# Performance work log

Hardware: AMD Instinct MI355X
Metric: run time of the kernel (lower is better)

Reference implementation:

```python
import jax, jax.numpy as jnp
import numpy as np

NUM_HEADS = 8
HEAD_SIZE = 64  # hidden_dim // num_heads = 512 // 8
SCALE = 1.0 / np.sqrt(HEAD_SIZE).astype(np.float32)
CAUSAL = True


def setup_inputs() -> dict:
    key = jax.random.key(0)
    k1, k2, k3 = jax.random.split(key, 3)
    b, s, d = 4, 2048, 512
    x = jax.random.normal(k1, (b, s, d), dtype=jnp.float32)
    w_qkv = jax.random.normal(k2, (d, 3 * d), dtype=jnp.float32) * 0.02
    b_qkv = jnp.zeros((3 * d,), dtype=jnp.float32)
    w_out = jax.random.normal(k3, (d, d), dtype=jnp.float32) * 0.02
    b_out = jnp.zeros((d,), dtype=jnp.float32)
    return {"x": x, "w_qkv": w_qkv, "b_qkv": b_qkv, "w_out": w_out, "b_out": b_out}


def reference(x, w_qkv, b_qkv, w_out, b_out):
    b, s, d = x.shape
    h, hd = NUM_HEADS, HEAD_SIZE
    qkv = x @ w_qkv + b_qkv                      # (b, s, 3d)
    q, k, v = jnp.split(qkv, 3, axis=-1)
    # (b, s, d) -> (b, h, s, hd)
    q = q.reshape(b, s, h, hd).transpose(0, 2, 1, 3)
    k = k.reshape(b, s, h, hd).transpose(0, 2, 1, 3)
    v = v.reshape(b, s, h, hd).transpose(0, 2, 1, 3)
    scores = jnp.einsum('bhqd,bhkd->bhqk', q, k) * SCALE  # (b, h, s, s)
    if CAUSAL:
        causal_mask = jnp.triu(jnp.ones((s, s), dtype=bool), k=1)
        scores = jnp.where(causal_mask, -jnp.inf, scores)
    attn = jax.nn.softmax(scores, axis=-1)
    out = jnp.einsum('bhqk,bhkd->bhqd', attn, v)          # (b, h, s, hd)
    out = out.transpose(0, 2, 1, 3).reshape(b, s, d)
    return out @ w_out + b_out
```

## Files before the change

kernel.cpp:

```cpp
#include <hip/hip_runtime.h>
#include <hip/hip_bf16.h>

#define BATCH 4
#define SEQ   2048
#define DM    512
#define NH    8
#define HD    64
#define PART  (BATCH*NH*SEQ*HD)
#define QSCALE 0.18033688f

typedef unsigned short u16;
typedef unsigned int   u32;
typedef __bf16 bf16x8 __attribute__((ext_vector_type(8)));
typedef float  f32x4  __attribute__((ext_vector_type(4)));

__device__ __forceinline__ u16 f2bf(float f) {
    union { float f; u32 u; } v; v.f = f;
    u32 r = v.u + 0x7fffu + ((v.u >> 16) & 1u);
    return (u16)(r >> 16);
}

__device__ __forceinline__ void glds16(const u16* g, u16* lds) {
    __builtin_amdgcn_global_load_lds(
        (const __attribute__((address_space(1))) void*)g,
        (__attribute__((address_space(3))) void*)lds, 16, 0, 0);
}

__global__ __launch_bounds__(256) void prep_k(
    const float* __restrict__ x, u16* __restrict__ xb,
    const float* __restrict__ w_qkv, u16* __restrict__ t_qkv,
    const float* __restrict__ w_out, u16* __restrict__ t_out)
{
    __shared__ u16 Ts[64][72];
    const int z = blockIdx.z, bx = blockIdx.x, t = threadIdx.x;

    if (z == 0) {
        const int n8 = PART / 8;
        for (int i = bx * 256 + t; i < n8; i += 512 * 256) {
            float4 a = *(const float4*)(x + (size_t)i * 8);
            float4 b = *(const float4*)(x + (size_t)i * 8 + 4);
            union { uint4 v; u16 s[8]; } o;
            o.s[0] = f2bf(a.x); o.s[1] = f2bf(a.y);
            o.s[2] = f2bf(a.z); o.s[3] = f2bf(a.w);
            o.s[4] = f2bf(b.x); o.s[5] = f2bf(b.y);
            o.s[6] = f2bf(b.z); o.s[7] = f2bf(b.w);
            *(uint4*)(xb + (size_t)i * 8) = o.v;
        }
        return;
    }
    const int N = (z == 1) ? 3 * DM : DM;
    const int ntiles = N / 64;
    if (bx >= ntiles * 8) return;
    const float* W = (z == 1) ? w_qkv : w_out;
    u16* Wt = (z == 1) ? t_qkv : t_out;
    const int n0 = (bx % ntiles) * 64, k0 = (bx / ntiles) * 64;

    #pragma unroll
    for (int l = 0; l < 4; ++l) {
        int idx = l * 1024 + t * 4;
        int r = idx >> 6, c = idx & 63;
        float4 v = *(const float4*)(W + (size_t)(k0 + r) * N + n0 + c);
        Ts[c + 0][r] = f2bf(v.x);
        Ts[c + 1][r] = f2bf(v.y);
        Ts[c + 2][r] = f2bf(v.z);
        Ts[c + 3][r] = f2bf(v.w);
    }
    __syncthreads();
    #pragma unroll
    for (int l = 0; l < 2; ++l) {
        int idx = l * 256 + t;
        int row = idx >> 3, ch = idx & 7;
        *(uint4*)(Wt + (size_t)(n0 + row) * DM + k0 + ch * 8) =
            *(const uint4*)(&Ts[row][ch * 8]);
    }
}

template<int MODE>
__global__ __launch_bounds__(256) void gemm_k(
    const u16* __restrict__ A, const u16* __restrict__ Bt,
    const float* __restrict__ bias, void* __restrict__ outv,
    int M, int N, int K)
{
    constexpr int BM = (MODE == 1) ? 64 : 128;
    constexpr int NI = (MODE == 1) ? 2 : 4;

    __shared__ __align__(16) u16 As[2][BM * 32];
    __shared__ __align__(16) u16 Bs[2][128 * 32];
    __shared__ __align__(16) u16 epi[128 * 72];

    const int tid  = threadIdx.x;
    const int bm0  = blockIdx.x * BM;
    const int bn0  = blockIdx.y * 128;
    const int wave = tid >> 6, lane = tid & 63;
    const int l16  = lane & 15, quad = lane >> 4;
    const int wr   = (MODE == 1) ? 0 : (wave & 1) * 64;
    const int wc   = (MODE == 1) ? wave * 32 : (wave >> 1) * 64;

    const int srow = (lane >> 2);
    const int scol = (lane & 3) * 8;
    const int arow = (MODE == 1) ? (wave * 16) : (wave * 32);
    const u16* Ag = A + (size_t)(bm0 + arow + srow) * K + scol;
    const u16* Bg = Bt + (size_t)(bn0 + wave * 32 + srow) * K + scol;
    const int wofsA = arow * 32;
    const int wofsB = (wave * 32) * 32;

    f32x4 acc[4][NI];
    #pragma unroll
    for (int i = 0; i < 4; ++i)
        #pragma unroll
        for (int j = 0; j < NI; ++j)
            acc[i][j] = (f32x4){0.f, 0.f, 0.f, 0.f};

    glds16(Ag, &As[0][wofsA]);
    if (MODE == 0) glds16(Ag + (size_t)16 * K, &As[0][wofsA + 16 * 32]);
    glds16(Bg,                  &Bs[0][wofsB]);
    glds16(Bg + (size_t)16 * K, &Bs[0][wofsB + 16 * 32]);
    __syncthreads();

    const int NIT = K >> 5;
    for (int it = 0; it < NIT; ++it) {
        const int cur = it & 1;
        if (it + 1 < NIT) {
            const int nx = cur ^ 1;
            const int k0 = (it + 1) << 5;
            glds16(Ag + k0, &As[nx][wofsA]);
            if (MODE == 0) glds16(Ag + k0 + (size_t)16 * K, &As[nx][wofsA + 16 * 32]);
            glds16(Bg + k0,                  &Bs[nx][wofsB]);
            glds16(Bg + k0 + (size_t)16 * K, &Bs[nx][wofsB + 16 * 32]);
        }

        bf16x8 af[4], bfr[NI];
        #pragma unroll
        for (int mi = 0; mi < 4; ++mi)
            af[mi] = *(const bf16x8*)(&As[cur][(wr + mi * 16 + l16) * 32 + quad * 8]);
        #pragma unroll
        for (int ni = 0; ni < NI; ++ni)
            bfr[ni] = *(const bf16x8*)(&Bs[cur][(wc + ni * 16 + l16) * 32 + quad * 8]);
        #pragma unroll
        for (int mi = 0; mi < 4; ++mi)
            #pragma unroll
            for (int ni = 0; ni < NI; ++ni)
                acc[mi][ni] = __builtin_amdgcn_mfma_f32_16x16x32_bf16(
                    af[mi], bfr[ni], acc[mi][ni], 0, 0, 0);
        __syncthreads();
    }

    if (MODE == 1) {
        #pragma unroll
        for (int mi = 0; mi < 4; ++mi)
            #pragma unroll
            for (int ni = 0; ni < NI; ++ni) {
                int col = bn0 + wc + ni * 16 + l16;
                float bv = bias[col];
                int row0 = bm0 + wr + mi * 16 + quad * 4;
                #pragma unroll
                for (int reg = 0; reg < 4; ++reg)
                    ((float*)outv)[(size_t)(row0 + reg) * N + col] =
                        acc[mi][ni][reg] + bv;
            }
    } else {
        u16* ws = (u16*)outv;
        const int part = bn0 >> 9;
        const int h0   = (bn0 & 511) >> 6;
        const int bq   = bm0 >> 11, s0 = bm0 & 2047;

        #pragma unroll
        for (int hh = 0; hh < 2; ++hh) {
            if ((wave >> 1) == hh) {
                #pragma unroll
                for (int mi = 0; mi < 4; ++mi)
                    #pragma unroll
                    for (int ni = 0; ni < 4; ++ni) {
                        int ce  = ni * 16 + l16;
                        float bv = bias[bn0 + wc + ce - 0];
                        int row0 = wr + mi * 16 + quad * 4;
                        if (part < 2) {
                            float scl = (part == 0) ? QSCALE : 1.0f;
                            #pragma unroll
                            for (int reg = 0; reg < 4; ++reg)
                                epi[(row0 + reg) * 72 + ce] =
                                    f2bf((acc[mi][ni][reg] + bv) * scl);
                        } else {
                            union { u16 q[4]; uint2 u; } pk;
                            #pragma unroll
                            for (int reg = 0; reg < 4; ++reg)
                                pk.q[reg] = f2bf(acc[mi][ni][reg] + bv);
                            *(uint2*)(&epi[ce * 144 + row0]) = pk.u;
                        }
                    }
            }
            __syncthreads();
            if (part < 2) {
                #pragma unroll
                for (int l = 0; l < 4; ++l) {
                    int idx = l * 256 + tid;
                    int r = idx >> 3, e8 = (idx & 7) * 8;
                    uint4 v = *(const uint4*)(&epi[r * 72 + e8]);
                    *(uint4*)(ws + (size_t)part * PART +
                              (((size_t)(bq * NH + h0 + hh) * SEQ) + s0 + r) * HD
                              + e8) = v;
                }
            } else {
                #pragma unroll
                for (int l = 0; l < 4; ++l) {
                    int idx = l * 256 + tid;
                    int e = idx >> 4, sc = (idx & 15) * 8;
                    uint4 v = *(const uint4*)(&epi[e * 144 + sc]);
                    *(uint4*)(ws + (size_t)2 * PART +
                              (((size_t)(bq * NH + h0 + hh) * HD) + e) * SEQ
                              + s0 + sc) = v;
                }
            }
            __syncthreads();
        }
    }
}

__global__ __launch_bounds__(256) void attn_k(
    const u16* __restrict__ Q, const u16* __restrict__ K,
    const u16* __restrict__ Vt, u16* __restrict__ O)
{
    __shared__ __align__(16) u16 KsB[2][64 * 64];
    __shared__ __align__(16) u16 VtB[3][64 * 64];
    __shared__ __align__(16) u16 Ps[2][64][72];

    const int bh = blockIdx.x;
    const int pair = blockIdx.y;
    const int tid = threadIdx.x, wave = tid >> 6, lane = tid & 63;
    const int l16 = lane & 15, quad = lane >> 4;
    const size_t baseK = (size_t)bh * SEQ * HD;
    const size_t baseV = (size_t)bh * HD * SEQ;
    const int b = bh >> 3, h = bh & 7;
    const int row64 = wave * 16 + quad * 4;

    const int sub = lane >> 3;
    const int lcx = (lane & 7) ^ sub;
    const u16* kg = K  + baseK + (size_t)((wave * 16 + sub) * 64)   + lcx * 8;
    const u16* vg = Vt + baseV + (size_t)((wave * 16 + sub) * 2048) + lcx * 8;
    u16* ksd = &KsB[0][wave * 1024];
    u16* vtd = &VtB[0][wave * 1024];

    #pragma unroll
    for (int phase = 0; phase < 2; ++phase) {
        const int qt = phase ? pair : (31 - pair);
        const size_t baseQ = baseK + (size_t)qt * 64 * HD;

        __syncthreads();

        #pragma unroll
        for (int r = 0; r < 2; ++r) {
            int chunk = r * 256 + tid;
            int row = chunk >> 3, c8 = (chunk & 7) << 3;
            *(uint4*)(&Ps[0][row][c8]) =
                *(const uint4*)(Q + baseQ + row * 64 + c8);
        }
        __syncthreads();
        bf16x8 qf[2];
        #pragma unroll
        for (int d0 = 0; d0 < 2; ++d0)
            qf[d0] = *(const bf16x8*)(&Ps[0][wave * 16 + l16][d0 * 32 + quad * 8]);

        glds16(kg,            ksd);
        glds16(kg + 8 * 64,   ksd + 512);
        glds16(vg,            vtd);
        glds16(vg + 8 * 2048, vtd + 512);
        __syncthreads();

        float l_part[4] = {0.f, 0.f, 0.f, 0.f};
        f32x4 o_acc[4];
        #pragma unroll
        for (int i = 0; i < 4; ++i) o_acc[i] = (f32x4){0.f, 0.f, 0.f, 0.f};

        for (int kt = 0; kt <= qt; ++kt) {
            if (kt < qt) {
                const int kx = ((kt + 1) & 1) * 4096;
                const int vx = ((kt + 1) % 3) * 4096;
                glds16(kg + (size_t)(kt + 1) * 4096,          ksd + kx);
                glds16(kg + (size_t)(kt + 1) * 4096 + 8 * 64, ksd + kx + 512);
                glds16(vg + (size_t)(kt + 1) * 64,            vtd + vx);
                glds16(vg + (size_t)(kt + 1) * 64 + 8 * 2048, vtd + vx + 512);
            }

            bf16x8 kf[2][4];
            #pragma unroll
            for (int d0 = 0; d0 < 2; ++d0)
                #pragma unroll
                for (int nt = 0; nt < 4; ++nt) {
                    int pc = (d0 * 4 + quad) ^ (l16 & 7);
                    kf[d0][nt] = *(const bf16x8*)
                        (&KsB[kt & 1][(nt * 16 + l16) * 64 + pc * 8]);
                }
            f32x4 s[4];
            #pragma unroll
            for (int nt = 0; nt < 4; ++nt) s[nt] = (f32x4){0.f, 0.f, 0.f, 0.f};
            #pragma unroll
            for (int d0 = 0; d0 < 2; ++d0)
                #pragma unroll
                for (int nt = 0; nt < 4; ++nt)
                    s[nt] = __builtin_amdgcn_mfma_f32_16x16x32_bf16(
                        qf[d0], kf[d0][nt], s[nt], 0, 0, 0);

            if (kt > 0) {
                const int pb = (kt - 1) & 1, vb = (kt - 1) % 3;
                bf16x8 vf[2][4];
                #pragma unroll
                for (int k0 = 0; k0 < 2; ++k0)
                    #pragma unroll
                    for (int dt = 0; dt < 4; ++dt) {
                        int pc = (k0 * 4 + quad) ^ (l16 & 7);
                        vf[k0][dt] = *(const bf16x8*)
                            (&VtB[vb][(dt * 16 + l16) * 64 + pc * 8]);
                    }
                #pragma unroll
                for (int k0 = 0; k0 < 2; ++k0) {
                    bf16x8 ap = *(const bf16x8*)
                        (&Ps[pb][wave * 16 + l16][k0 * 32 + quad * 8]);
                    #pragma unroll
                    for (int dt = 0; dt < 4; ++dt)
                        o_acc[dt] = __builtin_amdgcn_mfma_f32_16x16x32_bf16(
                            ap, vf[k0][dt], o_acc[dt], 0, 0, 0);
                }
            }

            const bool diag = (kt == qt);
            #pragma unroll
            for (int nt = 0; nt < 4; ++nt) {
                int cl = nt * 16 + l16;
                float p[4];
                #pragma unroll
                for (int reg = 0; reg < 4; ++reg) {
                    p[reg] = __builtin_amdgcn_exp2f(s[nt][reg]);
                    if (diag && cl > row64 + reg) p[reg] = 0.f;
                    l_part[reg] += p[reg];
                }
                union { __hip_bfloat162 hh2; u16 s2[2]; } pk01, pk23;
                pk01.hh2 = __float22bfloat162_rn(float2{p[0], p[1]});
                pk23.hh2 = __float22bfloat162_rn(float2{p[2], p[3]});
                Ps[kt & 1][row64 + 0][cl] = pk01.s2[0];
                Ps[kt & 1][row64 + 1][cl] = pk01.s2[1];
                Ps[kt & 1][row64 + 2][cl] = pk23.s2[0];
                Ps[kt & 1][row64 + 3][cl] = pk23.s2[1];
            }
            __syncthreads();
        }

        {
            const int pb = qt & 1, vb = qt % 3;
            bf16x8 vf[2][4];
            #pragma unroll
            for (int k0 = 0; k0 < 2; ++k0)
                #pragma unroll
                for (int dt = 0; dt < 4; ++dt) {
                    int pc = (k0 * 4 + quad) ^ (l16 & 7);
                    vf[k0][dt] = *(const bf16x8*)
                        (&VtB[vb][(dt * 16 + l16) * 64 + pc * 8]);
                }
            #pragma unroll
            for (int k0 = 0; k0 < 2; ++k0) {
                bf16x8 ap = *(const bf16x8*)
                    (&Ps[pb][wave * 16 + l16][k0 * 32 + quad * 8]);
                #pragma unroll
                for (int dt = 0; dt < 4; ++dt)
                    o_acc[dt] = __builtin_amdgcn_mfma_f32_16x16x32_bf16(
                        ap, vf[k0][dt], o_acc[dt], 0, 0, 0);
            }
        }

        float l_i[4];
        #pragma unroll
        for (int reg = 0; reg < 4; ++reg) {
            float l = l_part[reg];
            #pragma unroll
            for (int off = 1; off < 16; off <<= 1)
                l += __shfl_xor(l, off);
            l_i[reg] = l;
        }
        #pragma unroll
        for (int dt = 0; dt < 4; ++dt) {
            #pragma unroll
            for (int reg = 0; reg < 4; ++reg) {
                int srow = qt * 64 + row64 + reg;
                float v = o_acc[dt][reg] / l_i[reg];
                size_t idx = (((size_t)(b * SEQ + srow)) * NH + h) * HD
                             + dt * 16 + l16;
                O[idx] = f2bf(v);
            }
        }
    }
}

extern "C" void kernel_launch(void* const* d_in, const int* in_sizes, int n_in,
                              void* d_out, int out_size, void* d_ws, size_t ws_size,
                              hipStream_t stream) {
    const float* x     = (const float*)d_in[0];
    const float* w_qkv = (const float*)d_in[1];
    const float* b_qkv = (const float*)d_in[2];
    const float* w_out = (const float*)d_in[3];
    const float* b_out = (const float*)d_in[4];

    u16* qkv    = (u16*)d_ws;
    u16* attn   = qkv + (size_t)3 * PART;
    u16* xb     = attn + (size_t)PART;
    u16* wt_qkv = xb + (size_t)PART;
    u16* wt_out = wt_qkv + (size_t)(3 * DM) * DM;

    const int M = BATCH * SEQ;

    prep_k<<<dim3(512, 1, 3), 256, 0, stream>>>(x, xb, w_qkv, wt_qkv,
                                                w_out, wt_out);

    dim3 g1(M / 128, (3 * DM) / 128);
    gemm_k<0><<<g1, 256, 0, stream>>>(xb, wt_qkv, b_qkv, qkv, M, 3 * DM, DM);

    dim3 g2(BATCH * NH, 16);
    attn_k<<<g2, 256, 0, stream>>>(qkv, qkv + PART, qkv + 2 * (size_t)PART, attn);

    dim3 g3(M / 64, DM / 128);
    gemm_k<1><<<g3, 256, 0, stream>>>(attn, wt_out, b_out, (float*)d_out, M, DM, DM);
}
```

Before: 155.1 us.

## Shrink attention query tile to 32 rows with 2-wave blocks and simpler pipeline

The attention kernel now processes 32-row query tiles with 128-thread blocks, doubling the grid to 1024 blocks while keeping 64-wide KV tiles. The one-step software pipeline that deferred the P·V MFMA to the next iteration is removed: P·V is computed in the same iteration and V uses double buffering instead of triple. This is meant to raise occupancy and balance work across CUs on the causal workload and to cut LDS use. In exchange, each KV tile is loaded from global memory twice as often, and the softmax-to-PV dependency within an iteration is no longer hidden.

```diff
diff --git a/kernel.cpp b/kernel.cpp
--- a/kernel.cpp
+++ b/kernel.cpp
@@ -216,54 +216,55 @@
     }
 }
 
-__global__ __launch_bounds__(256) void attn_k(
+__global__ __launch_bounds__(128) void attn_k(
     const u16* __restrict__ Q, const u16* __restrict__ K,
     const u16* __restrict__ Vt, u16* __restrict__ O)
 {
     __shared__ __align__(16) u16 KsB[2][64 * 64];
-    __shared__ __align__(16) u16 VtB[3][64 * 64];
-    __shared__ __align__(16) u16 Ps[2][64][72];
+    __shared__ __align__(16) u16 VtB[2][64 * 64];
+    __shared__ __align__(16) u16 Ps[32][72];
 
     const int bh = blockIdx.x;
-    const int pair = blockIdx.y;
+    const int pr = blockIdx.y;
     const int tid = threadIdx.x, wave = tid >> 6, lane = tid & 63;
     const int l16 = lane & 15, quad = lane >> 4;
     const size_t baseK = (size_t)bh * SEQ * HD;
     const size_t baseV = (size_t)bh * HD * SEQ;
     const int b = bh >> 3, h = bh & 7;
-    const int row64 = wave * 16 + quad * 4;
+    const int row32 = wave * 16 + quad * 4;
 
     const int sub = lane >> 3;
     const int lcx = (lane & 7) ^ sub;
-    const u16* kg = K  + baseK + (size_t)((wave * 16 + sub) * 64)   + lcx * 8;
-    const u16* vg = Vt + baseV + (size_t)((wave * 16 + sub) * 2048) + lcx * 8;
-    u16* ksd = &KsB[0][wave * 1024];
-    u16* vtd = &VtB[0][wave * 1024];
+    const u16* kg = K  + baseK + (size_t)((wave * 32 + sub) * 64)   + lcx * 8;
+    const u16* vg = Vt + baseV + (size_t)((wave * 32 + sub) * 2048) + lcx * 8;
+    u16* ksd = &KsB[0][wave * 2048];
+    u16* vtd = &VtB[0][wave * 2048];
 
     #pragma unroll
     for (int phase = 0; phase < 2; ++phase) {
-        const int qt = phase ? pair : (31 - pair);
-        const size_t baseQ = baseK + (size_t)qt * 64 * HD;
+        const int t = phase ? pr : (63 - pr);
+        const int nkv = (t >> 1);
+        const size_t baseQ = baseK + (size_t)t * 32 * HD;
 
         __syncthreads();
 
         #pragma unroll
         for (int r = 0; r < 2; ++r) {
-            int chunk = r * 256 + tid;
-            int row = chunk >> 3, c8 = (chunk & 7) << 3;
-            *(uint4*)(&Ps[0][row][c8]) =
-                *(const uint4*)(Q + baseQ + row * 64 + c8);
+            int idx = r * 128 + tid;
+            int row = idx >> 3, c8 = (idx & 7) << 3;
+            *(uint4*)(&Ps[row][c8]) = *(const uint4*)(Q + baseQ + row * 64 + c8);
         }
         __syncthreads();
         bf16x8 qf[2];
         #pragma unroll
         for (int d0 = 0; d0 < 2; ++d0)
-            qf[d0] = *(const bf16x8*)(&Ps[0][wave * 16 + l16][d0 * 32 + quad * 8]);
-
-        glds16(kg,            ksd);
-        glds16(kg + 8 * 64,   ksd + 512);
-        glds16(vg,            vtd);
-        glds16(vg + 8 * 2048, vtd + 512);
+            qf[d0] = *(const bf16x8*)(&Ps[wave * 16 + l16][d0 * 32 + quad * 8]);
+
+        #pragma unroll
+        for (int i = 0; i < 4; ++i) {
+            glds16(kg + (size_t)i * 8 * 64,   ksd + i * 512);
+            glds16(vg + (size_t)i * 8 * 2048, vtd + i * 512);
+        }
         __syncthreads();
 
         float l_part[4] = {0.f, 0.f, 0.f, 0.f};
@@ -271,25 +272,31 @@
         #pragma unroll
         for (int i = 0; i < 4; ++i) o_acc[i] = (f32x4){0.f, 0.f, 0.f, 0.f};
 
-        for (int kt = 0; kt <= qt; ++kt) {
-            if (kt < qt) {
-                const int kx = ((kt + 1) & 1) * 4096;
-                const int vx = ((kt + 1) % 3) * 4096;
-                glds16(kg + (size_t)(kt + 1) * 4096,          ksd + kx);
-                glds16(kg + (size_t)(kt + 1) * 4096 + 8 * 64, ksd + kx + 512);
-                glds16(vg + (size_t)(kt + 1) * 64,            vtd + vx);
-                glds16(vg + (size_t)(kt + 1) * 64 + 8 * 2048, vtd + vx + 512);
-            }
-
-            bf16x8 kf[2][4];
+        for (int kt = 0; kt <= nkv; ++kt) {
+            const int cur = kt & 1;
+            if (kt < nkv) {
+                const int nx = (cur ^ 1) * 4096;
+                #pragma unroll
+                for (int i = 0; i < 4; ++i) {
+                    glds16(kg + (size_t)(kt + 1) * 4096 + (size_t)i * 8 * 64,
+                           ksd + nx + i * 512);
+                    glds16(vg + (size_t)(kt + 1) * 64 + (size_t)i * 8 * 2048,
+                           vtd + nx + i * 512);
+                }
+            }
+
+            bf16x8 kf[2][4], vf[2][4];
             #pragma unroll
             for (int d0 = 0; d0 < 2; ++d0)
                 #pragma unroll
                 for (int nt = 0; nt < 4; ++nt) {
                     int pc = (d0 * 4 + quad) ^ (l16 & 7);
                     kf[d0][nt] = *(const bf16x8*)
-                        (&KsB[kt & 1][(nt * 16 + l16) * 64 + pc * 8]);
-                }
+                        (&KsB[cur][(nt * 16 + l16) * 64 + pc * 8]);
+                    vf[d0][nt] = *(const bf16x8*)
+                        (&VtB[cur][(nt * 16 + l16) * 64 + pc * 8]);
+                }
+
             f32x4 s[4];
             #pragma unroll
             for (int nt = 0; nt < 4; ++nt) s[nt] = (f32x4){0.f, 0.f, 0.f, 0.f};
@@ -300,29 +307,8 @@
                     s[nt] = __builtin_amdgcn_mfma_f32_16x16x32_bf16(
                         qf[d0], kf[d0][nt], s[nt], 0, 0, 0);
 
-            if (kt > 0) {
-                const int pb = (kt - 1) & 1, vb = (kt - 1) % 3;
-                bf16x8 vf[2][4];
-                #pragma unroll
-                for (int k0 = 0; k0 < 2; ++k0)
-                    #pragma unroll
-                    for (int dt = 0; dt < 4; ++dt) {
-                        int pc = (k0 * 4 + quad) ^ (l16 & 7);
-                        vf[k0][dt] = *(const bf16x8*)
-                            (&VtB[vb][(dt * 16 + l16) * 64 + pc * 8]);
-                    }
-                #pragma unroll
-                for (int k0 = 0; k0 < 2; ++k0) {
-                    bf16x8 ap = *(const bf16x8*)
-                        (&Ps[pb][wave * 16 + l16][k0 * 32 + quad * 8]);
-                    #pragma unroll
-                    for (int dt = 0; dt < 4; ++dt)
-                        o_acc[dt] = __builtin_amdgcn_mfma_f32_16x16x32_bf16(
-                            ap, vf[k0][dt], o_acc[dt], 0, 0, 0);
-                }
-            }
-
-            const bool diag = (kt == qt);
+            const bool diag = (kt == nkv);
+            const int rbase = (t & 1) * 32 + row32;
             #pragma unroll
             for (int nt = 0; nt < 4; ++nt) {
                 int cl = nt * 16 + l16;
@@ -330,40 +316,28 @@
                 #pragma unroll
                 for (int reg = 0; reg < 4; ++reg) {
                     p[reg] = __builtin_amdgcn_exp2f(s[nt][reg]);
-                    if (diag && cl > row64 + reg) p[reg] = 0.f;
+                    if (diag && cl > rbase + reg) p[reg] = 0.f;
                     l_part[reg] += p[reg];
                 }
                 union { __hip_bfloat162 hh2; u16 s2[2]; } pk01, pk23;
                 pk01.hh2 = __float22bfloat162_rn(float2{p[0], p[1]});
                 pk23.hh2 = __float22bfloat162_rn(float2{p[2], p[3]});
-                Ps[kt & 1][row64 + 0][cl] = pk01.s2[0];
-                Ps[kt & 1][row64 + 1][cl] = pk01.s2[1];
-                Ps[kt & 1][row64 + 2][cl] = pk23.s2[0];
-                Ps[kt & 1][row64 + 3][cl] = pk23.s2[1];
-            }
-            __syncthreads();
-        }
-
-        {
-            const int pb = qt & 1, vb = qt % 3;
-            bf16x8 vf[2][4];
-            #pragma unroll
-            for (int k0 = 0; k0 < 2; ++k0)
-                #pragma unroll
-                for (int dt = 0; dt < 4; ++dt) {
-                    int pc = (k0 * 4 + quad) ^ (l16 & 7);
-                    vf[k0][dt] = *(const bf16x8*)
-                        (&VtB[vb][(dt * 16 + l16) * 64 + pc * 8]);
-                }
+                Ps[row32 + 0][cl] = pk01.s2[0];
+                Ps[row32 + 1][cl] = pk01.s2[1];
+                Ps[row32 + 2][cl] = pk23.s2[0];
+                Ps[row32 + 3][cl] = pk23.s2[1];
+            }
+
             #pragma unroll
             for (int k0 = 0; k0 < 2; ++k0) {
                 bf16x8 ap = *(const bf16x8*)
-                    (&Ps[pb][wave * 16 + l16][k0 * 32 + quad * 8]);
+                    (&Ps[wave * 16 + l16][k0 * 32 + quad * 8]);
                 #pragma unroll
                 for (int dt = 0; dt < 4; ++dt)
                     o_acc[dt] = __builtin_amdgcn_mfma_f32_16x16x32_bf16(
                         ap, vf[k0][dt], o_acc[dt], 0, 0, 0);
             }
+            __syncthreads();
         }
 
         float l_i[4];
@@ -379,7 +353,7 @@
         for (int dt = 0; dt < 4; ++dt) {
             #pragma unroll
             for (int reg = 0; reg < 4; ++reg) {
-                int srow = qt * 64 + row64 + reg;
+                int srow = t * 32 + row32 + reg;
                 float v = o_acc[dt][reg] / l_i[reg];
                 size_t idx = (((size_t)(b * SEQ + srow)) * NH + h) * HD
                              + dt * 16 + l16;
@@ -412,8 +386,8 @@
     dim3 g1(M / 128, (3 * DM) / 128);
     gemm_k<0><<<g1, 256, 0, stream>>>(xb, wt_qkv, b_qkv, qkv, M, 3 * DM, DM);
 
-    dim3 g2(BATCH * NH, 16);
-    attn_k<<<g2, 256, 0, stream>>>(qkv, qkv + PART, qkv + 2 * (size_t)PART, attn);
+    dim3 g2(BATCH * NH, 32);
+    attn_k<<<g2, 128, 0, stream>>>(qkv, qkv + PART, qkv + 2 * (size_t)PART, attn);
 
     dim3 g3(M / 64, DM / 128);
     gemm_k<1><<<g3, 256, 0, stream>>>(attn, wt_out, b_out, (float*)d_out, M, DM, DM);
```

Result: no change. 157.0 us (+1.2%).

## Fuse x fp32-to-bf16 conversion into QKV GEMM and unpipeline attention PV

Applied to the files above, without the earlier changes.

Removes the separate x-to-bf16 pass from the prep kernel. The QKV GEMM now loads fp32 x directly, converts it in registers and stores bf16 into LDS, which saves writing and re-reading the bf16 copy of x in global memory. The GEMM template is split into two specialized kernels. In attention, the PV MFMA for each tile now runs in the same iteration as its QK instead of one iteration later, so V and P need only double and single buffering. This cuts LDS use but removes the overlap between softmax and the previous tile's PV work.

```diff
diff --git a/kernel.cpp b/kernel.cpp
--- a/kernel.cpp
+++ b/kernel.cpp
@@ -19,6 +19,11 @@
     u32 r = v.u + 0x7fffu + ((v.u >> 16) & 1u);
     return (u16)(r >> 16);
 }
+__device__ __forceinline__ u32 pk2(float a, float b) {
+    union { __hip_bfloat162 h; u32 u; } x;
+    x.h = __float22bfloat162_rn(float2{a, b});
+    return x.u;
+}
 
 __device__ __forceinline__ void glds16(const u16* g, u16* lds) {
     __builtin_amdgcn_global_load_lds(
@@ -27,33 +32,16 @@
 }
 
 __global__ __launch_bounds__(256) void prep_k(
-    const float* __restrict__ x, u16* __restrict__ xb,
     const float* __restrict__ w_qkv, u16* __restrict__ t_qkv,
     const float* __restrict__ w_out, u16* __restrict__ t_out)
 {
     __shared__ u16 Ts[64][72];
-    const int z = blockIdx.z, bx = blockIdx.x, t = threadIdx.x;
-
-    if (z == 0) {
-        const int n8 = PART / 8;
-        for (int i = bx * 256 + t; i < n8; i += 512 * 256) {
-            float4 a = *(const float4*)(x + (size_t)i * 8);
-            float4 b = *(const float4*)(x + (size_t)i * 8 + 4);
-            union { uint4 v; u16 s[8]; } o;
-            o.s[0] = f2bf(a.x); o.s[1] = f2bf(a.y);
-            o.s[2] = f2bf(a.z); o.s[3] = f2bf(a.w);
-            o.s[4] = f2bf(b.x); o.s[5] = f2bf(b.y);
-            o.s[6] = f2bf(b.z); o.s[7] = f2bf(b.w);
-            *(uint4*)(xb + (size_t)i * 8) = o.v;
-        }
-        return;
-    }
-    const int N = (z == 1) ? 3 * DM : DM;
-    const int ntiles = N / 64;
-    if (bx >= ntiles * 8) return;
-    const float* W = (z == 1) ? w_qkv : w_out;
-    u16* Wt = (z == 1) ? t_qkv : t_out;
-    const int n0 = (bx % ntiles) * 64, k0 = (bx / ntiles) * 64;
+    const int bx = blockIdx.x, t = threadIdx.x;
+    const float* W; u16* Wt; int N, n0, k0;
+    if (bx < 192) { W = w_qkv; Wt = t_qkv; N = 3 * DM;
+                    n0 = (bx % 24) * 64; k0 = (bx / 24) * 64; }
+    else          { int i = bx - 192; W = w_out; Wt = t_out; N = DM;
+                    n0 = (i % 8) * 64;  k0 = (i / 8) * 64; }
 
     #pragma unroll
     for (int l = 0; l < 4; ++l) {
@@ -75,44 +63,174 @@
     }
 }
 
-template<int MODE>
-__global__ __launch_bounds__(256) void gemm_k(
-    const u16* __restrict__ A, const u16* __restrict__ Bt,
-    const float* __restrict__ bias, void* __restrict__ outv,
-    int M, int N, int K)
+__global__ __launch_bounds__(256) void gemm_qkv_k(
+    const float* __restrict__ A, const u16* __restrict__ Bt,
+    const float* __restrict__ bias, u16* __restrict__ ws)
 {
-    constexpr int BM = (MODE == 1) ? 64 : 128;
-    constexpr int NI = (MODE == 1) ? 2 : 4;
-
-    __shared__ __align__(16) u16 As[2][BM * 32];
+    constexpr int K = DM;
+    __shared__ __align__(16) u16 As[2][128 * 32];
     __shared__ __align__(16) u16 Bs[2][128 * 32];
     __shared__ __align__(16) u16 epi[128 * 72];
 
     const int tid  = threadIdx.x;
-    const int bm0  = blockIdx.x * BM;
+    const int bm0  = blockIdx.x * 128;
     const int bn0  = blockIdx.y * 128;
     const int wave = tid >> 6, lane = tid & 63;
     const int l16  = lane & 15, quad = lane >> 4;
-    const int wr   = (MODE == 1) ? 0 : (wave & 1) * 64;
-    const int wc   = (MODE == 1) ? wave * 32 : (wave >> 1) * 64;
-
-    const int srow = (lane >> 2);
-    const int scol = (lane & 3) * 8;
-    const int arow = (MODE == 1) ? (wave * 16) : (wave * 32);
-    const u16* Ag = A + (size_t)(bm0 + arow + srow) * K + scol;
+    const int wr   = (wave & 1) * 64;
+    const int wc   = (wave >> 1) * 64;
+
+    const int arow = tid >> 1, acol = (tid & 1) * 16;
+    const float* Ax = A + (size_t)(bm0 + arow) * K + acol;
+    f32x4 ar[4];
+
+    const int srow = (lane >> 2), scol = (lane & 3) * 8;
     const u16* Bg = Bt + (size_t)(bn0 + wave * 32 + srow) * K + scol;
-    const int wofsA = arow * 32;
     const int wofsB = (wave * 32) * 32;
 
-    f32x4 acc[4][NI];
+    f32x4 acc[4][4];
     #pragma unroll
     for (int i = 0; i < 4; ++i)
         #pragma unroll
-        for (int j = 0; j < NI; ++j)
+        for (int j = 0; j < 4; ++j)
             acc[i][j] = (f32x4){0.f, 0.f, 0.f, 0.f};
 
-    glds16(Ag, &As[0][wofsA]);
-    if (MODE == 0) glds16(Ag + (size_t)16 * K, &As[0][wofsA + 16 * 32]);
+    #pragma unroll
+    for (int i = 0; i < 4; ++i)
+        ar[i] = *(const f32x4*)(Ax + i * 4);
+    {
+        uint4 w0 = {pk2(ar[0][0], ar[0][1]), pk2(ar[0][2], ar[0][3]),
+                    pk2(ar[1][0], ar[1][1]), pk2(ar[1][2], ar[1][3])};
+        uint4 w1 = {pk2(ar[2][0], ar[2][1]), pk2(ar[2][2], ar[2][3]),
+                    pk2(ar[3][0], ar[3][1]), pk2(ar[3][2], ar[3][3])};
+        *(uint4*)(&As[0][arow * 32 + acol])     = w0;
+        *(uint4*)(&As[0][arow * 32 + acol + 8]) = w1;
+    }
+    glds16(Bg,                  &Bs[0][wofsB]);
+    glds16(Bg + (size_t)16 * K, &Bs[0][wofsB + 16 * 32]);
+    __syncthreads();
+
+    const int NIT = K >> 5;
+    for (int it = 0; it < NIT; ++it) {
+        const int cur = it & 1, nx = cur ^ 1;
+        if (it + 1 < NIT) {
+            const int k0 = (it + 1) << 5;
+            #pragma unroll
+            for (int i = 0; i < 4; ++i)
+                ar[i] = *(const f32x4*)(Ax + k0 + i * 4);
+            glds16(Bg + k0,                  &Bs[nx][wofsB]);
+            glds16(Bg + k0 + (size_t)16 * K, &Bs[nx][wofsB + 16 * 32]);
+        }
+
+        bf16x8 af[4], bfr[4];
+        #pragma unroll
+        for (int mi = 0; mi < 4; ++mi)
+            af[mi] = *(const bf16x8*)(&As[cur][(wr + mi * 16 + l16) * 32 + quad * 8]);
+        #pragma unroll
+        for (int ni = 0; ni < 4; ++ni)
+            bfr[ni] = *(const bf16x8*)(&Bs[cur][(wc + ni * 16 + l16) * 32 + quad * 8]);
+        #pragma unroll
+        for (int mi = 0; mi < 4; ++mi)
+            #pragma unroll
+            for (int ni = 0; ni < 4; ++ni)
+                acc[mi][ni] = __builtin_amdgcn_mfma_f32_16x16x32_bf16(
+                    af[mi], bfr[ni], acc[mi][ni], 0, 0, 0);
+
+        if (it + 1 < NIT) {
+            uint4 w0 = {pk2(ar[0][0], ar[0][1]), pk2(ar[0][2], ar[0][3]),
+                        pk2(ar[1][0], ar[1][1]), pk2(ar[1][2], ar[1][3])};
+            uint4 w1 = {pk2(ar[2][0], ar[2][1]), pk2(ar[2][2], ar[2][3]),
+                        pk2(ar[3][0], ar[3][1]), pk2(ar[3][2], ar[3][3])};
+            *(uint4*)(&As[nx][arow * 32 + acol])     = w0;
+            *(uint4*)(&As[nx][arow * 32 + acol + 8]) = w1;
+        }
+        __syncthreads();
+    }
+
+    const int part = bn0 >> 9;
+    const int h0   = (bn0 & 511) >> 6;
+    const int bq   = bm0 >> 11, s0 = bm0 & 2047;
+
+    #pragma unroll
+    for (int hh = 0; hh < 2; ++hh) {
+        if ((wave >> 1) == hh) {
+            #pragma unroll
+            for (int mi = 0; mi < 4; ++mi)
+                #pragma unroll
+                for (int ni = 0; ni < 4; ++ni) {
+                    int ce  = ni * 16 + l16;
+                    float bv = bias[bn0 + hh * 64 + ce];
+                    int row0 = wr + mi * 16 + quad * 4;
+                    if (part < 2) {
+                        float scl = (part == 0) ? QSCALE : 1.0f;
+                        #pragma unroll
+                        for (int reg = 0; reg < 4; ++reg)
+                            epi[(row0 + reg) * 72 + ce] =
+                                f2bf((acc[mi][ni][reg] + bv) * scl);
+                    } else {
+                        union { u16 q[4]; uint2 u; } pk;
+                        #pragma unroll
+                        for (int reg = 0; reg < 4; ++reg)
+                            pk.q[reg] = f2bf(acc[mi][ni][reg] + bv);
+                        *(uint2*)(&epi[ce * 144 + row0]) = pk.u;
+                    }
+                }
+        }
+        __syncthreads();
+        if (part < 2) {
+            #pragma unroll
+            for (int l = 0; l < 4; ++l) {
+                int idx = l * 256 + tid;
+                int r = idx >> 3, e8 = (idx & 7) * 8;
+                uint4 v = *(const uint4*)(&epi[r * 72 + e8]);
+                *(uint4*)(ws + (size_t)part * PART +
+                          (((size_t)(bq * NH + h0 + hh) * SEQ) + s0 + r) * HD
+                          + e8) = v;
+            }
+        } else {
+            #pragma unroll
+            for (int l = 0; l < 4; ++l) {
+                int idx = l * 256 + tid;
+                int e = idx >> 4, sc = (idx & 15) * 8;
+                uint4 v = *(const uint4*)(&epi[e * 144 + sc]);
+                *(uint4*)(ws + (size_t)2 * PART +
+                          (((size_t)(bq * NH + h0 + hh) * HD) + e) * SEQ
+                          + s0 + sc) = v;
+            }
+        }
+        __syncthreads();
+    }
+}
+
+__global__ __launch_bounds__(256) void gemm_out_k(
+    const u16* __restrict__ A, const u16* __restrict__ Bt,
+    const float* __restrict__ bias, float* __restrict__ out)
+{
+    constexpr int K = DM, N = DM;
+    __shared__ __align__(16) u16 As[2][64 * 32];
+    __shared__ __align__(16) u16 Bs[2][128 * 32];
+
+    const int tid  = threadIdx.x;
+    const int bm0  = blockIdx.x * 64;
+    const int bn0  = blockIdx.y * 128;
+    const int wave = tid >> 6, lane = tid & 63;
+    const int l16  = lane & 15, quad = lane >> 4;
+    const int wc   = wave * 32;
+
+    const int srow = (lane >> 2), scol = (lane & 3) * 8;
+    const u16* Ag = A + (size_t)(bm0 + wave * 16 + srow) * K + scol;
+    const u16* Bg = Bt + (size_t)(bn0 + wave * 32 + srow) * K + scol;
+    const int wofsA = (wave * 16) * 32;
+    const int wofsB = (wave * 32) * 32;
+
+    f32x4 acc[4][2];
+    #pragma unroll
+    for (int i = 0; i < 4; ++i)
+        #pragma unroll
+        for (int j = 0; j < 2; ++j)
+            acc[i][j] = (f32x4){0.f, 0.f, 0.f, 0.f};
+
+    glds16(Ag,                  &As[0][wofsA]);
     glds16(Bg,                  &Bs[0][wofsB]);
     glds16(Bg + (size_t)16 * K, &Bs[0][wofsB + 16 * 32]);
     __syncthreads();
@@ -123,97 +241,38 @@
         if (it + 1 < NIT) {
             const int nx = cur ^ 1;
             const int k0 = (it + 1) << 5;
-            glds16(Ag + k0, &As[nx][wofsA]);
-            if (MODE == 0) glds16(Ag + k0 + (size_t)16 * K, &As[nx][wofsA + 16 * 32]);
+            glds16(Ag + k0,                  &As[nx][wofsA]);
             glds16(Bg + k0,                  &Bs[nx][wofsB]);
             glds16(Bg + k0 + (size_t)16 * K, &Bs[nx][wofsB + 16 * 32]);
         }
 
-        bf16x8 af[4], bfr[NI];
+        bf16x8 af[4], bfr[2];
         #pragma unroll
         for (int mi = 0; mi < 4; ++mi)
-            af[mi] = *(const bf16x8*)(&As[cur][(wr + mi * 16 + l16) * 32 + quad * 8]);
-        #pragma unroll
-        for (int ni = 0; ni < NI; ++ni)
+            af[mi] = *(const bf16x8*)(&As[cur][(mi * 16 + l16) * 32 + quad * 8]);
+        #pragma unroll
+        for (int ni = 0; ni < 2; ++ni)
             bfr[ni] = *(const bf16x8*)(&Bs[cur][(wc + ni * 16 + l16) * 32 + quad * 8]);
         #pragma unroll
         for (int mi = 0; mi < 4; ++mi)
             #pragma unroll
-            for (int ni = 0; ni < NI; ++ni)
+            for (int ni = 0; ni < 2; ++ni)
                 acc[mi][ni] = __builtin_amdgcn_mfma_f32_16x16x32_bf16(
                     af[mi], bfr[ni], acc[mi][ni], 0, 0, 0);
         __syncthreads();
     }
 
-    if (MODE == 1) {
-        #pragma unroll
-        for (int mi = 0; mi < 4; ++mi)
-            #pragma unroll
-            for (int ni = 0; ni < NI; ++ni) {
-                int col = bn0 + wc + ni * 16 + l16;
-                float bv = bias[col];
-                int row0 = bm0 + wr + mi * 16 + quad * 4;
-                #pragma unroll
-                for (int reg = 0; reg < 4; ++reg)
-                    ((float*)outv)[(size_t)(row0 + reg) * N + col] =
-                        acc[mi][ni][reg] + bv;
-            }
-    } else {
-        u16* ws = (u16*)outv;
-        const int part = bn0 >> 9;
-        const int h0   = (bn0 & 511) >> 6;
-        const int bq   = bm0 >> 11, s0 = bm0 & 2047;
-
-        #pragma unroll
-        for (int hh = 0; hh < 2; ++hh) {
-            if ((wave >> 1) == hh) {
-                #pragma unroll
-                for (int mi = 0; mi < 4; ++mi)
-                    #pragma unroll
-                    for (int ni = 0; ni < 4; ++ni) {
-                        int ce  = ni * 16 + l16;
-                        float bv = bias[bn0 + wc + ce - 0];
-                        int row0 = wr + mi * 16 + quad * 4;
-                        if (part < 2) {
-                            float scl = (part == 0) ? QSCALE : 1.0f;
-                            #pragma unroll
-                            for (int reg = 0; reg < 4; ++reg)
-                                epi[(row0 + reg) * 72 + ce] =
-                                    f2bf((acc[mi][ni][reg] + bv) * scl);
-                        } else {
-                            union { u16 q[4]; uint2 u; } pk;
-                            #pragma unroll
-                            for (int reg = 0; reg < 4; ++reg)
-                                pk.q[reg] = f2bf(acc[mi][ni][reg] + bv);
-                            *(uint2*)(&epi[ce * 144 + row0]) = pk.u;
-                        }
-                    }
-            }
-            __syncthreads();
-            if (part < 2) {
-                #pragma unroll
-                for (int l = 0; l < 4; ++l) {
-                    int idx = l * 256 + tid;
-                    int r = idx >> 3, e8 = (idx & 7) * 8;
-                    uint4 v = *(const uint4*)(&epi[r * 72 + e8]);
-                    *(uint4*)(ws + (size_t)part * PART +
-                              (((size_t)(bq * NH + h0 + hh) * SEQ) + s0 + r) * HD
-                              + e8) = v;
-                }
-            } else {
-                #pragma unroll
-                for (int l = 0; l < 4; ++l) {
-                    int idx = l * 256 + tid;
-                    int e = idx >> 4, sc = (idx & 15) * 8;
-                    uint4 v = *(const uint4*)(&epi[e * 144 + sc]);
-                    *(uint4*)(ws + (size_t)2 * PART +
-                              (((size_t)(bq * NH + h0 + hh) * HD) + e) * SEQ
-                              + s0 + sc) = v;
-                }
-            }
-            __syncthreads();
-        }
-    }
+    #pragma unroll
+    for (int mi = 0; mi < 4; ++mi)
+        #pragma unroll
+        for (int ni = 0; ni < 2; ++ni) {
+            int col = bn0 + wc + ni * 16 + l16;
+            float bv = bias[col];
+            int row0 = bm0 + mi * 16 + quad * 4;
+            #pragma unroll
+            for (int reg = 0; reg < 4; ++reg)
+                out[(size_t)(row0 + reg) * N + col] = acc[mi][ni][reg] + bv;
+        }
 }
 
 __global__ __launch_bounds__(256) void attn_k(
@@ -221,8 +280,8 @@
     const u16* __restrict__ Vt, u16* __restrict__ O)
 {
     __shared__ __align__(16) u16 KsB[2][64 * 64];
-    __shared__ __align__(16) u16 VtB[3][64 * 64];
-    __shared__ __align__(16) u16 Ps[2][64][72];
+    __shared__ __align__(16) u16 VtB[2][64 * 64];
+    __shared__ __align__(16) u16 Ps[64][72];
 
     const int bh = blockIdx.x;
     const int pair = blockIdx.y;
@@ -251,14 +310,13 @@
         for (int r = 0; r < 2; ++r) {
             int chunk = r * 256 + tid;
             int row = chunk >> 3, c8 = (chunk & 7) << 3;
-            *(uint4*)(&Ps[0][row][c8]) =
-                *(const uint4*)(Q + baseQ + row * 64 + c8);
+            *(uint4*)(&Ps[row][c8]) = *(const uint4*)(Q + baseQ + row * 64 + c8);
         }
         __syncthreads();
         bf16x8 qf[2];
         #pragma unroll
         for (int d0 = 0; d0 < 2; ++d0)
-            qf[d0] = *(const bf16x8*)(&Ps[0][wave * 16 + l16][d0 * 32 + quad * 8]);
+            qf[d0] = *(const bf16x8*)(&Ps[wave * 16 + l16][d0 * 32 + quad * 8]);
 
         glds16(kg,            ksd);
         glds16(kg + 8 * 64,   ksd + 512);
@@ -272,24 +330,27 @@
         for (int i = 0; i < 4; ++i) o_acc[i] = (f32x4){0.f, 0.f, 0.f, 0.f};
 
         for (int kt = 0; kt <= qt; ++kt) {
+            const int cur = kt & 1;
             if (kt < qt) {
-                const int kx = ((kt + 1) & 1) * 4096;
-                const int vx = ((kt + 1) % 3) * 4096;
-                glds16(kg + (size_t)(kt + 1) * 4096,          ksd + kx);
-                glds16(kg + (size_t)(kt + 1) * 4096 + 8 * 64, ksd + kx + 512);
-                glds16(vg + (size_t)(kt + 1) * 64,            vtd + vx);
-                glds16(vg + (size_t)(kt + 1) * 64 + 8 * 2048, vtd + vx + 512);
-            }
-
-            bf16x8 kf[2][4];
+                const int nx = (cur ^ 1) * 4096;
+                glds16(kg + (size_t)(kt + 1) * 4096,          ksd + nx);
+                glds16(kg + (size_t)(kt + 1) * 4096 + 8 * 64, ksd + nx + 512);
+                glds16(vg + (size_t)(kt + 1) * 64,            vtd + nx);
+                glds16(vg + (size_t)(kt + 1) * 64 + 8 * 2048, vtd + nx + 512);
+            }
+
+            bf16x8 kf[2][4], vf[2][4];
             #pragma unroll
             for (int d0 = 0; d0 < 2; ++d0)
                 #pragma unroll
                 for (int nt = 0; nt < 4; ++nt) {
                     int pc = (d0 * 4 + quad) ^ (l16 & 7);
                     kf[d0][nt] = *(const bf16x8*)
-                        (&KsB[kt & 1][(nt * 16 + l16) * 64 + pc * 8]);
+                        (&KsB[cur][(nt * 16 + l16) * 64 + pc * 8]);
+                    vf[d0][nt] = *(const bf16x8*)
+                        (&VtB[cur][(nt * 16 + l16) * 64 + pc * 8]);
                 }
+
             f32x4 s[4];
             #pragma unroll
             for (int nt = 0; nt < 4; ++nt) s[nt] = (f32x4){0.f, 0.f, 0.f, 0.f};
@@ -299,28 +360,6 @@
                 for (int nt = 0; nt < 4; ++nt)
                     s[nt] = __builtin_amdgcn_mfma_f32_16x16x32_bf16(
                         qf[d0], kf[d0][nt], s[nt], 0, 0, 0);
-
-            if (kt > 0) {
-                const int pb = (kt - 1) & 1, vb = (kt - 1) % 3;
-                bf16x8 vf[2][4];
-                #pragma unroll
-                for (int k0 = 0; k0 < 2; ++k0)
-                    #pragma unroll
-                    for (int dt = 0; dt < 4; ++dt) {
-                        int pc = (k0 * 4 + quad) ^ (l16 & 7);
-                        vf[k0][dt] = *(const bf16x8*)
-                            (&VtB[vb][(dt * 16 + l16) * 64 + pc * 8]);
-                    }
-                #pragma unroll
-                for (int k0 = 0; k0 < 2; ++k0) {
-                    bf16x8 ap = *(const bf16x8*)
-                        (&Ps[pb][wave * 16 + l16][k0 * 32 + quad * 8]);
-                    #pragma unroll
-                    for (int dt = 0; dt < 4; ++dt)
-                        o_acc[dt] = __builtin_amdgcn_mfma_f32_16x16x32_bf16(
-                            ap, vf[k0][dt], o_acc[dt], 0, 0, 0);
-                }
-            }
 
             const bool diag = (kt == qt);
             #pragma unroll
@@ -336,34 +375,22 @@
                 union { __hip_bfloat162 hh2; u16 s2[2]; } pk01, pk23;
                 pk01.hh2 = __float22bfloat162_rn(float2{p[0], p[1]});
                 pk23.hh2 = __float22bfloat162_rn(float2{p[2], p[3]});
-                Ps[kt & 1][row64 + 0][cl] = pk01.s2[0];
-                Ps[kt & 1][row64 + 1][cl] = pk01.s2[1];
-                Ps[kt & 1][row64 + 2][cl] = pk23.s2[0];
-                Ps[kt & 1][row64 + 3][cl] = pk23.s2[1];
-            }
-            __syncthreads();
-        }
-
-        {
-            const int pb = qt & 1, vb = qt % 3;
-            bf16x8 vf[2][4];
-            #pragma unroll
-            for (int k0 = 0; k0 < 2; ++k0)
-                #pragma unroll
-                for (int dt = 0; dt < 4; ++dt) {
-                    int pc = (k0 * 4 + quad) ^ (l16 & 7);
-                    vf[k0][dt] = *(const bf16x8*)
-                        (&VtB[vb][(dt * 16 + l16) * 64 + pc * 8]);
-                }
+                Ps[row64 + 0][cl] = pk01.s2[0];
+                Ps[row64 + 1][cl] = pk01.s2[1];
+                Ps[row64 + 2][cl] = pk23.s2[0];
+                Ps[row64 + 3][cl] = pk23.s2[1];
+            }
+
             #pragma unroll
             for (int k0 = 0; k0 < 2; ++k0) {
                 bf16x8 ap = *(const bf16x8*)
-                    (&Ps[pb][wave * 16 + l16][k0 * 32 + quad * 8]);
+                    (&Ps[wave * 16 + l16][k0 * 32 + quad * 8]);
                 #pragma unroll
                 for (int dt = 0; dt < 4; ++dt)
                     o_acc[dt] = __builtin_amdgcn_mfma_f32_16x16x32_bf16(
                         ap, vf[k0][dt], o_acc[dt], 0, 0, 0);
             }
+            __syncthreads();
         }
 
         float l_i[4];
@@ -400,21 +427,19 @@
 
     u16* qkv    = (u16*)d_ws;
     u16* attn   = qkv + (size_t)3 * PART;
-    u16* xb     = attn + (size_t)PART;
-    u16* wt_qkv = xb + (size_t)PART;
+    u16* wt_qkv = attn + (size_t)PART;
     u16* wt_out = wt_qkv + (size_t)(3 * DM) * DM;
 
     const int M = BATCH * SEQ;
 
-    prep_k<<<dim3(512, 1, 3), 256, 0, stream>>>(x, xb, w_qkv, wt_qkv,
-                                                w_out, wt_out);
+    prep_k<<<256, 256, 0, stream>>>(w_qkv, wt_qkv, w_out, wt_out);
 
     dim3 g1(M / 128, (3 * DM) / 128);
-    gemm_k<0><<<g1, 256, 0, stream>>>(xb, wt_qkv, b_qkv, qkv, M, 3 * DM, DM);
+    gemm_qkv_k<<<g1, 256, 0, stream>>>(x, wt_qkv, b_qkv, qkv);
 
     dim3 g2(BATCH * NH, 16);
     attn_k<<<g2, 256, 0, stream>>>(qkv, qkv + PART, qkv + 2 * (size_t)PART, attn);
 
     dim3 g3(M / 64, DM / 128);
-    gemm_k<1><<<g3, 256, 0, stream>>>(attn, wt_out, b_out, (float*)d_out, M, DM, DM);
-}
+    gemm_out_k<<<g3, 256, 0, stream>>>(attn, wt_out, b_out, (float*)d_out);
+}
```

Result: no change. 154.4 us (-0.5%).
